# Kernel optimization log

Measured on AMD Instinct MI355X. Metric: run time of the kernel, lower is better.

The kernel has to match this reference:

```python
import jax, jax.numpy as jnp
import numpy as np

EPS_LN = 1e-5

def _layernorm(x, g, b):
    mu = jnp.mean(x, axis=-1, keepdims=True)
    var = jnp.mean((x - mu) ** 2, axis=-1, keepdims=True)
    return (x - mu) * jax.lax.rsqrt(var + EPS_LN) * g + b


def setup_inputs() -> dict:
    B, S, D = 8, 2048, 512
    key = jax.random.key(0)
    ks = jax.random.split(key, 12)
    s = 1.0 / np.sqrt(D)
    inp = {
        "x": jax.random.normal(ks[0], (B, S, D), dtype=jnp.float32),
        "ln1_g": jnp.ones((D,), jnp.float32),
        "ln1_b": jnp.zeros((D,), jnp.float32),
        "ln2_g": jnp.ones((D,), jnp.float32),
        "ln2_b": jnp.zeros((D,), jnp.float32),
        "Wq": jax.random.normal(ks[1], (D, D), jnp.float32) * s,
        "bq": jnp.zeros((D,), jnp.float32),
        "Wk": jax.random.normal(ks[2], (D, D), jnp.float32) * s,
        "bk": jnp.zeros((D,), jnp.float32),
        "Wv": jax.random.normal(ks[3], (D, D), jnp.float32) * s,
        "bv": jnp.zeros((D,), jnp.float32),
        "Wi": jax.random.normal(ks[4], (D, D), jnp.float32) * s,
        "bi": jnp.zeros((D,), jnp.float32),
        "Wf": jax.random.normal(ks[5], (D, D), jnp.float32) * s,
        "bf": jnp.zeros((D,), jnp.float32),
        "Wo": jax.random.normal(ks[6], (D, D), jnp.float32) * s,
        "bo": jnp.zeros((D,), jnp.float32),
        "W1": jax.random.normal(ks[7], (D, 4 * D), jnp.float32) * s,
        "b1": jnp.zeros((4 * D,), jnp.float32),
        "W2": jax.random.normal(ks[8], (4 * D, D), jnp.float32) * (1.0 / np.sqrt(4 * D)),
        "b2": jnp.zeros((D,), jnp.float32),
    }
    return inp


def reference(x, ln1_g, ln1_b, ln2_g, ln2_b, Wq, bq, Wk, bk, Wv, bv,
              Wi, bi, Wf, bf, Wo, bo, W1, b1, W2, b2):
    B, S, D = x.shape
    normed = _layernorm(x, ln1_g, ln1_b)                      # [B,S,D]
    # All projections depend only on x -> batch them over time.
    q = normed @ Wq + bq
    k = (normed @ Wk + bk) / jnp.sqrt(jnp.float32(D))
    v = normed @ Wv + bv
    it = normed @ Wi + bi
    ft = normed @ Wf + bf
    o = jax.nn.sigmoid(normed @ Wo + bo)

    def tm(a):  # time-major [S,B,D]
        return jnp.swapaxes(a, 0, 1)

    def step(carry, xs):
        C, n, m = carry
        q_t, k_t, v_t, it_t, ft_t, o_t = xs
        m_new = jnp.maximum(ft_t + m, it_t)
        i_g = jnp.exp(it_t - m_new)
        f_g = jnp.exp(ft_t + m - m_new)
        # outer(v,k): [B,D,1]*[B,1,D]
        C_new = f_g[..., None] * C + i_g[..., None] * (v_t[:, :, None] * k_t[:, None, :])
        n_new = f_g * n + i_g * k_t
        h = o_t * jnp.einsum('bij,bj->bi', C_new, q_t)
        return (C_new, n_new, m_new), h

    C0 = jnp.zeros((B, D, D), x.dtype)
    n0 = jnp.zeros((B, D), x.dtype)
    m0 = jnp.zeros((B, D), x.dtype)
    (_, _, _), h_seq = jax.lax.scan(step, (C0, n0, m0),
                                    (tm(q), tm(k), tm(v), tm(it), tm(ft), tm(o)))
    h = jnp.swapaxes(h_seq, 0, 1)                             # [B,S,D]

    out = x + h
    ffn_in = _layernorm(out, ln2_g, ln2_b)
    ffn = jax.nn.gelu(ffn_in @ W1 + b1, approximate=False) @ W2 + b2
    return out + ffn
```

## Files before the change

### kernel.cpp

```cpp
#include <hip/hip_runtime.h>
#include <hip/hip_bf16.h>
#include <cstdint>

typedef unsigned short u16;
typedef unsigned int u32;
typedef __attribute__((ext_vector_type(8))) short short8;
typedef __attribute__((ext_vector_type(4))) float f32x4;

#define NB 8
#define NS 2048
#define ND 512
#define NM (NB * NS)
#define CL 64
#define NCH (NS / CL)
static constexpr size_t BSDn = (size_t)NM * ND;
#define KSCALE 0.044194173824159216f

#define OFF_QB ((size_t)0)
#define OFF_KB (BSDn * 2)
#define OFF_KT (BSDn * 4)
#define OFF_VT (BSDn * 6)
#define OFF_OT (BSDn * 8)
#define OFF_IT (BSDn * 10)
#define OFF_FT (BSDn * 14)
#define OFF_G  (BSDn * 18)
#define OFF_AC (BSDn * 18 + ((size_t)2 << 20))
#define OFF_X  (OFF_AC + ((size_t)32 << 20))
#define OFF_UB (OFF_X + ((size_t)16 << 20))
#define OFF_GA (OFF_UB + ((size_t)16 << 20))
#define OFF_END (OFF_GA + ((size_t)1 << 20))

typedef __attribute__((address_space(1))) const u32 gas_u32;
typedef __attribute__((address_space(3))) u32 las_u32;

__device__ __forceinline__ u16 f2bf(float f) {
    u32 i = __builtin_bit_cast(u32, f);
    u32 r = i + 0x7FFFu + ((i >> 16) & 1u);
    return (u16)(r >> 16);
}
__device__ __forceinline__ float bf2f(u16 h) {
    return __builtin_bit_cast(float, (u32)h << 16);
}

__device__ __forceinline__ void lds_barrier() {
    __builtin_amdgcn_sched_barrier(0);
    asm volatile("s_waitcnt lgkmcnt(0)" ::: "memory");
    __builtin_amdgcn_s_barrier();
    __builtin_amdgcn_sched_barrier(0);
}

__global__ __launch_bounds__(256) void wcorr_kernel(
        const float* __restrict__ Wi, const float* __restrict__ Wf,
        u16* __restrict__ WT) {
    int idx = blockIdx.x * 256 + threadIdx.x;
    int n = idx / 1536, k = idx - n * 1536;
    const float* Wp = (n >> 9) ? Wf : Wi;
    int d = n & 511;
    u16 o;
    if (k < 1024) {
        o = f2bf(Wp[(size_t)(k & 511) * 512 + d]);
    } else {
        float w = Wp[(size_t)(k - 1024) * 512 + d];
        o = f2bf(w - bf2f(f2bf(w)));
    }
    WT[idx] = o;
}

__global__ __launch_bounds__(256) void wconv_kernel(const float* __restrict__ W,
        u16* __restrict__ WT, int lk, int N, int total) {
    int idx = blockIdx.x * 256 + threadIdx.x;
    if (idx >= total) return;
    int n = idx >> lk;
    int k = idx & ((1 << lk) - 1);
    WT[idx] = f2bf(W[(size_t)k * N + n]);
}

__global__ __launch_bounds__(256) void bias_concat_kernel(
        const float* b0, const float* b1, const float* b2,
        const float* b3, const float* b4, const float* b5,
        float* __restrict__ ball) {
    int idx = blockIdx.x * 256 + threadIdx.x;
    if (idx >= 3072) return;
    int p = idx >> 9, d = idx & 511;
    float v;
    switch (p) {
        case 0: v = b0[d]; break;
        case 1: v = b1[d]; break;
        case 2: v = b2[d]; break;
        case 3: v = b3[d]; break;
        case 4: v = b4[d]; break;
        default: v = b5[d]; break;
    }
    ball[idx] = v;
}

__global__ __launch_bounds__(256) void ln1_kernel(const float* __restrict__ x,
        const float* __restrict__ g, const float* __restrict__ bb,
        u16* __restrict__ nout) {
    int wave = threadIdx.x >> 6, lane = threadIdx.x & 63;
    size_t row = (size_t)blockIdx.x * 4 + wave;
    const float* xr = x + row * ND + lane * 8;
    float4 a0 = *(const float4*)xr;
    float4 a1 = *(const float4*)(xr + 4);
    float xs[8] = {a0.x, a0.y, a0.z, a0.w, a1.x, a1.y, a1.z, a1.w};
    float s = 0.f;
#pragma unroll
    for (int u = 0; u < 8; ++u) s += xs[u];
#pragma unroll
    for (int off = 32; off; off >>= 1) s += __shfl_xor(s, off);
    float mu = s * (1.0f / ND);
    float ss = 0.f;
#pragma unroll
    for (int u = 0; u < 8; ++u) { xs[u] -= mu; ss += xs[u] * xs[u]; }
#pragma unroll
    for (int off = 32; off; off >>= 1) ss += __shfl_xor(ss, off);
    float rs = rsqrtf(ss * (1.0f / ND) + 1e-5f);
    const float* gp = g + lane * 8;
    const float* bp = bb + lane * 8;
    float4 g0 = *(const float4*)gp, g1 = *(const float4*)(gp + 4);
    float4 c0 = *(const float4*)bp, c1 = *(const float4*)(bp + 4);
    float gg[8] = {g0.x, g0.y, g0.z, g0.w, g1.x, g1.y, g1.z, g1.w};
    float cc[8] = {c0.x, c0.y, c0.z, c0.w, c1.x, c1.y, c1.z, c1.w};
    u32 owh[4], owl[4];
#pragma unroll
    for (int u = 0; u < 4; ++u) {
        float y0 = xs[2 * u] * rs * gg[2 * u] + cc[2 * u];
        float y1 = xs[2 * u + 1] * rs * gg[2 * u + 1] + cc[2 * u + 1];
        u16 h0 = f2bf(y0), h1 = f2bf(y1);
        u16 l0 = f2bf(y0 - bf2f(h0)), l1 = f2bf(y1 - bf2f(h1));
        owh[u] = (u32)h0 | ((u32)h1 << 16);
        owl[u] = (u32)l0 | ((u32)l1 << 16);
    }
    u16* rb = nout + row * 1024;
    *(uint4*)(rb + lane * 8) = make_uint4(owh[0], owh[1], owh[2], owh[3]);
    *(uint4*)(rb + 512 + lane * 8) = make_uint4(owl[0], owl[1], owl[2], owl[3]);
}

__global__ __launch_bounds__(256) void resid_ln2_kernel(const float* __restrict__ x,
        const float* __restrict__ h, const float* __restrict__ g,
        const float* __restrict__ bb, float* __restrict__ outb,
        u16* __restrict__ fin) {
    int wave = threadIdx.x >> 6, lane = threadIdx.x & 63;
    size_t row = (size_t)blockIdx.x * 4 + wave;
    const float* xr = x + row * ND + lane * 8;
    const float* hr = h + row * ND + lane * 8;
    float4 a0 = *(const float4*)xr;
    float4 a1 = *(const float4*)(xr + 4);
    float4 h0 = *(const float4*)hr;
    float4 h1 = *(const float4*)(hr + 4);
    float xs[8] = {a0.x + h0.x, a0.y + h0.y, a0.z + h0.z, a0.w + h0.w,
                   a1.x + h1.x, a1.y + h1.y, a1.z + h1.z, a1.w + h1.w};
    float* orow = outb + row * ND + lane * 8;
    *(float4*)orow = make_float4(xs[0], xs[1], xs[2], xs[3]);
    *(float4*)(orow + 4) = make_float4(xs[4], xs[5], xs[6], xs[7]);
    float s = 0.f;
#pragma unroll
    for (int u = 0; u < 8; ++u) s += xs[u];
#pragma unroll
    for (int off = 32; off; off >>= 1) s += __shfl_xor(s, off);
    float mu = s * (1.0f / ND);
    float ss = 0.f;
#pragma unroll
    for (int u = 0; u < 8; ++u) { xs[u] -= mu; ss += xs[u] * xs[u]; }
#pragma unroll
    for (int off = 32; off; off >>= 1) ss += __shfl_xor(ss, off);
    float rs = rsqrtf(ss * (1.0f / ND) + 1e-5f);
    const float* gp = g + lane * 8;
    const float* bp = bb + lane * 8;
    float4 g0 = *(const float4*)gp, g1 = *(const float4*)(gp + 4);
    float4 c0 = *(const float4*)bp, c1 = *(const float4*)(bp + 4);
    float gg[8] = {g0.x, g0.y, g0.z, g0.w, g1.x, g1.y, g1.z, g1.w};
    float cc[8] = {c0.x, c0.y, c0.z, c0.w, c1.x, c1.y, c1.z, c1.w};
    u32 ow[4];
#pragma unroll
    for (int u = 0; u < 4; ++u) {
        float y0 = xs[2 * u] * rs * gg[2 * u] + cc[2 * u];
        float y1 = xs[2 * u + 1] * rs * gg[2 * u + 1] + cc[2 * u + 1];
        ow[u] = (u32)f2bf(y0) | ((u32)f2bf(y1) << 16);
    }
    *(uint4*)(fin + row * ND + lane * 8) = make_uint4(ow[0], ow[1], ow[2], ow[3]);
}

__global__ __launch_bounds__(256) void gqk_kernel(
        const u16* __restrict__ Qb, const u16* __restrict__ Kb,
        u16* __restrict__ Gm) {
    __shared__ u16 Qs[64][520];
    __shared__ u16 Ks[64][520];
    int tid = threadIdx.x;
    int w = tid >> 6, lane = tid & 63;
    int b = blockIdx.x >> 5, c = blockIdx.x & 31;
    int t0 = c * CL;
    {
        int row = tid >> 2, cb = (tid & 3) * 128;
        const u16* qsrc = Qb + ((size_t)b * NS + t0 + row) * ND + cb;
        const u16* ksrc = Kb + ((size_t)b * NS + t0 + row) * ND + cb;
#pragma unroll
        for (int u = 0; u < 16; ++u) {
            *(short8*)&Qs[row][cb + u * 8] = *(const short8*)(qsrc + u * 8);
            *(short8*)&Ks[row][cb + u * 8] = *(const short8*)(ksrc + u * 8);
        }
    }
    __syncthreads();
    int qw = lane & 15, kg = lane >> 4;
    f32x4 ga[4];
#pragma unroll
    for (int ns = 0; ns < 4; ++ns) ga[ns] = (f32x4){0.f, 0.f, 0.f, 0.f};
    for (int kb = 0; kb < 16; ++kb) {
        short8 aq = *(const short8*)&Qs[(w << 4) + qw][kb * 32 + (kg << 3)];
#pragma unroll
        for (int ns = 0; ns < 4; ++ns) {
            short8 bk = *(const short8*)&Ks[(ns << 4) + qw][kb * 32 + (kg << 3)];
            ga[ns] = __builtin_amdgcn_mfma_f32_16x16x32_bf16(aq, bk, ga[ns], 0, 0, 0);
        }
    }
    u16* gout = Gm + (size_t)(b * NCH + c) * CL * CL;
#pragma unroll
    for (int ns = 0; ns < 4; ++ns) {
#pragma unroll
        for (int rg = 0; rg < 4; ++rg) {
            int t = (w << 4) + (kg << 2) + rg;
            int s = (ns << 4) + qw;
            gout[t * CL + s] = (s <= t) ? f2bf(ga[ns][rg]) : (u16)0;
        }
    }
}

__global__ __launch_bounds__(128) void gates_kernel(
        const float* __restrict__ IT, const float* __restrict__ FT,
        const u16* __restrict__ VT,
        u16* __restrict__ A1g, u16* __restrict__ A2g,
        u16* __restrict__ Ubg, float* __restrict__ gamg) {
    int w = threadIdx.x >> 6, lane = threadIdx.x & 63;
    int rp = blockIdx.x & 7;
    int bl = blockIdx.x >> 3;
    int b = bl >> 5, isl = bl & 31;
    int il = rp * 2 + w;
    int i = (isl << 4) + il;
    size_t rowb = ((size_t)b * ND + i) * NS;
    size_t tb = (size_t)bl * 32 * 1024 + il * 64;
    float mo = 0.f;
    for (int c = 0; c < NCH; ++c) {
        size_t gofs = rowb + c * CL + lane;
        float ft = FT[gofs];
        float it = IT[gofs];
        float vv = bf2f(VT[gofs]);
        float bs = ft;
#pragma unroll
        for (int o = 1; o < 64; o <<= 1) {
            float nv = __shfl_up(bs, o);
            if (lane >= o) bs += nv;
        }
        float e = it - bs;
        float Mv = e;
#pragma unroll
        for (int o = 1; o < 64; o <<= 1) {
            float nv = __shfl_up(Mv, o);
            if (lane >= o) Mv = fmaxf(Mv, nv);
        }
        Mv = fmaxf(Mv, mo);
        float E = __shfl(Mv, 63);
        size_t oofs = tb + (size_t)c * 1024 + lane;
        Ubg[oofs] = f2bf(__expf(e - E) * vv);
        A1g[oofs] = f2bf(__expf(mo - Mv));
        A2g[oofs] = f2bf(__expf(fminf(E - Mv, 80.f)));
        if (lane == 0) gamg[((size_t)bl * 32 + c) * 16 + il] = __expf(mo - E);
        float bs63 = __shfl(bs, 63);
        mo = bs63 + E;
    }
}

__global__ __launch_bounds__(512) void recur_kernel(
        const u16* __restrict__ Qb, const u16* __restrict__ KT,
        const u16* __restrict__ Gm,
        const u16* __restrict__ A1g, const u16* __restrict__ A2g,
        const u16* __restrict__ Ubg, const float* __restrict__ gamg,
        const u16* __restrict__ OT, float* __restrict__ H) {
    __shared__ u16 Chi[2][16][520];
    __shared__ u16 Ubl[2][16][72];
    __shared__ u16 A1l[2][16][66];
    __shared__ u16 A2l[2][16][66];
    __shared__ float gaml[2][16];
    int tid = threadIdx.x;
    int w = tid >> 6, lane = tid & 63;
    int tt = w & 3, half = w >> 2;
    int b = blockIdx.x & 7;
    int isl = blockIdx.x >> 3;
    int i0 = isl << 4;
    int qw = lane & 15, kg = lane >> 4;
    f32x4 cacc[4];
#pragma unroll
    for (int n = 0; n < 4; ++n) cacc[n] = (f32x4){0.f, 0.f, 0.f, 0.f};

    size_t bT = (size_t)b * NS;
    size_t bD = (size_t)b * ND;
    size_t gtile = (size_t)(b * 32 + isl) * 32 * 1024;
    int srow = tid >> 5, spair = (tid & 31) << 1;

    const u16* qpf = Qb + (bT + (tt << 4) + qw) * ND + (kg << 3);
    const u16* kpf = KT + (bD + (w << 6) + qw) * NS + (kg << 3);
    const u16* gpf = Gm + ((size_t)(b * NCH) * CL + (tt << 4) + qw) * CL + (kg << 3);
    const u16* ubp = Ubg + gtile + srow * 64 + spair;
    const u16* a1p = A1g + gtile + srow * 64 + spair;
    const u16* a2p = A2g + gtile + srow * 64 + spair;
    const float* gamp = gamg + (size_t)(b * 32 + isl) * 512 + tid;
    const u16* otp = OT + (bD + i0 + qw) * NS + (tt << 4) + (kg << 2);

    u32 nub = 0, na1 = 0, na2 = 0;
    float ngam = 0.f;
    uint2 nov = make_uint2(0, 0);
    short8 nq[16], nk[8], ng[2];

    auto issue_gates = [&]() {
        nub = *(const u32*)ubp; ubp += 1024;
        na1 = *(const u32*)a1p; a1p += 1024;
        na2 = *(const u32*)a2p; a2p += 1024;
        if (tid < 16) ngam = *gamp;
        gamp += 16;
    };
    auto issue_big = [&]() {
        if (half == 0) {
#pragma unroll
            for (int kk = 0; kk < 16; ++kk)
                nq[kk] = *(const short8*)(qpf + kk * 32);
            ng[0] = *(const short8*)gpf;
            ng[1] = *(const short8*)(gpf + 32);
            nov = *(const uint2*)otp;
        }
        qpf += CL * ND;
        gpf += CL * CL;
        otp += CL;
#pragma unroll
        for (int kb = 0; kb < 2; ++kb)
#pragma unroll
            for (int n = 0; n < 4; ++n)
                nk[kb * 4 + n] = *(const short8*)(kpf + (size_t)(n << 4) * NS + kb * 32);
        kpf += CL;
    };

    issue_gates();
    issue_big();
    for (int c = 0; c < NCH; ++c) {
        int buf = c & 1;
        int t0 = c * CL;
        u32 cub = nub, ca1 = na1, ca2 = na2;
        float cgam = ngam;
        uint2 cov = nov;
        if (c + 1 < NCH) issue_gates();

        *(u32*)&Ubl[buf][srow][spair] = cub;
        *(u32*)&A1l[buf][srow][spair] = ca1;
        *(u32*)&A2l[buf][srow][spair] = ca2;
        if (tid < 16) gaml[buf][tid] = cgam;
#pragma unroll
        for (int n = 0; n < 4; ++n) {
            int j = (w << 6) + (n << 4) + qw;
#pragma unroll
            for (int rg = 0; rg < 4; ++rg)
                Chi[buf][(kg << 2) + rg][j] = f2bf(cacc[n][rg]);
        }
        lds_barrier();

        f32x4 qc0 = (f32x4){0.f, 0.f, 0.f, 0.f};
        f32x4 qc1 = (f32x4){0.f, 0.f, 0.f, 0.f};
        f32x4 pin = (f32x4){0.f, 0.f, 0.f, 0.f};
        if (half == 0) {
#pragma unroll
            for (int kk = 0; kk < 8; ++kk) {
                short8 b0 = *(const short8*)&Chi[buf][qw][(2 * kk) * 32 + (kg << 3)];
                short8 b1 = *(const short8*)&Chi[buf][qw][(2 * kk + 1) * 32 + (kg << 3)];
                qc0 = __builtin_amdgcn_mfma_f32_16x16x32_bf16(nq[2 * kk], b0, qc0, 0, 0, 0);
                qc1 = __builtin_amdgcn_mfma_f32_16x16x32_bf16(nq[2 * kk + 1], b1, qc1, 0, 0, 0);
            }
#pragma unroll
            for (int kb = 0; kb < 2; ++kb) {
                short8 bu = *(const short8*)&Ubl[buf][qw][kb * 32 + (kg << 3)];
                pin = __builtin_amdgcn_mfma_f32_16x16x32_bf16(ng[kb], bu, pin, 0, 0, 0);
            }
        }
        {
            float g[4];
#pragma unroll
            for (int rg = 0; rg < 4; ++rg) g[rg] = gaml[buf][(kg << 2) + rg];
#pragma unroll
            for (int n = 0; n < 4; ++n) {
#pragma unroll
                for (int rg = 0; rg < 4; ++rg) cacc[n][rg] *= g[rg];
            }
#pragma unroll
            for (int kb = 0; kb < 2; ++kb) {
                short8 au = *(const short8*)&Ubl[buf][qw][kb * 32 + (kg << 3)];
#pragma unroll
                for (int n = 0; n < 4; ++n)
                    cacc[n] = __builtin_amdgcn_mfma_f32_16x16x32_bf16(
                            au, nk[kb * 4 + n], cacc[n], 0, 0, 0);
            }
        }
        float a1v[4], a2v[4];
        if (half == 0) {
#pragma unroll
            for (int rg = 0; rg < 4; ++rg) {
                int tl = (tt << 4) + (kg << 2) + rg;
                a1v[rg] = bf2f(A1l[buf][qw][tl]);
                a2v[rg] = bf2f(A2l[buf][qw][tl]);
            }
        }
        if (c + 1 < NCH) issue_big();
        if (half == 0) {
            float ov[4];
            ov[0] = bf2f((u16)(cov.x & 0xffff));
            ov[1] = bf2f((u16)(cov.x >> 16));
            ov[2] = bf2f((u16)(cov.y & 0xffff));
            ov[3] = bf2f((u16)(cov.y >> 16));
#pragma unroll
            for (int rg = 0; rg < 4; ++rg) {
                int tl = (tt << 4) + (kg << 2) + rg;
                float qc = qc0[rg] + qc1[rg];
                H[(bT + t0 + tl) * ND + i0 + qw] = ov[rg] * (a1v[rg] * qc + a2v[rg] * pin[rg]);
            }
        }
    }
}

template <int MODE>
__global__ __launch_bounds__(256) void gemm_kernel(
        const u16* __restrict__ A, const u16* __restrict__ BT,
        int M, int N, int K, int lda, int ldb, int kwrap,
        const float* __restrict__ bias,
        char* __restrict__ pb,
        float* __restrict__ outf, u16* __restrict__ outh,
        const float* __restrict__ resid) {
    __shared__ u16 As[2][128 * 32];
    __shared__ u16 Bs[2][128 * 32];
    int tid = threadIdx.x;
    int wave = tid >> 6, lane = tid & 63;
    int wm = wave >> 1, wn = wave & 1;
    int m0 = blockIdx.y * 128;
    int n0 = blockIdx.x * 128;

    f32x4 acc[4][4];
#pragma unroll
    for (int fi = 0; fi < 4; ++fi)
#pragma unroll
        for (int fj = 0; fj < 4; ++fj)
            acc[fi][fj] = (f32x4){0.f, 0.f, 0.f, 0.f};

    int srow = lane >> 2;
    int slot = lane & 3;
    int r0s = wave * 32 + srow;
    int gs0 = (slot ^ ((r0s >> 1) & 3)) << 3;
    int gs1 = (slot ^ (((r0s + 16) >> 1) & 3)) << 3;
    const u16* Ag0 = A + (size_t)(m0 + r0s) * lda + gs0;
    const u16* Ag1 = A + (size_t)(m0 + r0s + 16) * lda + gs1;
    const u16* Bg0 = BT + (size_t)(n0 + r0s) * ldb + gs0;
    const u16* Bg1 = BT + (size_t)(n0 + r0s + 16) * ldb + gs1;
    int wl0 = wave * 32 * 32;
    int wl1 = wl0 + 16 * 32;

    int fr = lane & 15, kb = lane >> 4;
    int ra[4], rb4[4], sa[4], sb[4];
#pragma unroll
    for (int f = 0; f < 4; ++f) {
        ra[f] = wm * 64 + f * 16 + fr;
        rb4[f] = wn * 64 + f * 16 + fr;
        sa[f] = ra[f] * 32 + ((kb ^ ((ra[f] >> 1) & 3)) << 3);
        sb[f] = rb4[f] * 32 + ((kb ^ ((rb4[f] >> 1) & 3)) << 3);
    }

    int nk = K >> 5;
    __builtin_amdgcn_global_load_lds((gas_u32*)Ag0, (las_u32*)(&As[0][wl0]), 16, 0, 0);
    __builtin_amdgcn_global_load_lds((gas_u32*)Ag1, (las_u32*)(&As[0][wl1]), 16, 0, 0);
    __builtin_amdgcn_global_load_lds((gas_u32*)Bg0, (las_u32*)(&Bs[0][wl0]), 16, 0, 0);
    __builtin_amdgcn_global_load_lds((gas_u32*)Bg1, (las_u32*)(&Bs[0][wl1]), 16, 0, 0);
    __syncthreads();
#pragma unroll 2
    for (int t = 0; t < nk; ++t) {
        int cur = t & 1;
        if (t + 1 < nk) {
            int k0 = (t + 1) << 5;
            int ak0 = k0 - (k0 >= kwrap ? kwrap : 0);
            __builtin_amdgcn_global_load_lds((gas_u32*)(Ag0 + ak0), (las_u32*)(&As[cur ^ 1][wl0]), 16, 0, 0);
            __builtin_amdgcn_global_load_lds((gas_u32*)(Ag1 + ak0), (las_u32*)(&As[cur ^ 1][wl1]), 16, 0, 0);
            __builtin_amdgcn_global_load_lds((gas_u32*)(Bg0 + k0), (las_u32*)(&Bs[cur ^ 1][wl0]), 16, 0, 0);
            __builtin_amdgcn_global_load_lds((gas_u32*)(Bg1 + k0), (las_u32*)(&Bs[cur ^ 1][wl1]), 16, 0, 0);
        }
        short8 fa[4], fb[4];
#pragma unroll
        for (int f = 0; f < 4; ++f) {
            fa[f] = *(const short8*)(&As[cur][sa[f]]);
            fb[f] = *(const short8*)(&Bs[cur][sb[f]]);
        }
#pragma unroll
        for (int fi = 0; fi < 4; ++fi)
#pragma unroll
            for (int fj = 0; fj < 4; ++fj)
                acc[fi][fj] = __builtin_amdgcn_mfma_f32_16x16x32_bf16(
                        fa[fi], fb[fj], acc[fi][fj], 0, 0, 0);
        __syncthreads();
    }

    int rbase = (lane >> 4) * 4;
    int cbase = n0 + wn * 64 + (lane & 15);
#pragma unroll
    for (int fi = 0; fi < 4; ++fi) {
        int r0 = m0 + wm * 64 + fi * 16 + rbase;
#pragma unroll
        for (int fj = 0; fj < 4; ++fj) {
            int col = cbase + fj * 16;
            if (MODE == 0) {
                int p = col >> 9, d = col & 511;
                float bv_ = bias[col];
                float w0 = acc[fi][fj][0] + bv_;
                float w1 = acc[fi][fj][1] + bv_;
                float w2 = acc[fi][fj][2] + bv_;
                float w3 = acc[fi][fj][3] + bv_;
                size_t tb = ((size_t)(r0 >> 11) * ND + d) * NS + (r0 & 2047);
                if (p == 0) {
                    u16* q = (u16*)(pb + OFF_QB);
                    q[(size_t)(r0 + 0) * ND + d] = f2bf(w0);
                    q[(size_t)(r0 + 1) * ND + d] = f2bf(w1);
                    q[(size_t)(r0 + 2) * ND + d] = f2bf(w2);
                    q[(size_t)(r0 + 3) * ND + d] = f2bf(w3);
                } else if (p == 1) {
                    float s0 = w0 * KSCALE, s1 = w1 * KSCALE;
                    float s2 = w2 * KSCALE, s3 = w3 * KSCALE;
                    u16* kbuf = (u16*)(pb + OFF_KB);
                    kbuf[(size_t)(r0 + 0) * ND + d] = f2bf(s0);
                    kbuf[(size_t)(r0 + 1) * ND + d] = f2bf(s1);
                    kbuf[(size_t)(r0 + 2) * ND + d] = f2bf(s2);
                    kbuf[(size_t)(r0 + 3) * ND + d] = f2bf(s3);
                    uint2 wv = make_uint2((u32)f2bf(s0) | ((u32)f2bf(s1) << 16),
                                          (u32)f2bf(s2) | ((u32)f2bf(s3) << 16));
                    *(uint2*)((u16*)(pb + OFF_KT) + tb) = wv;
                } else if (p == 2) {
                    uint2 wv = make_uint2((u32)f2bf(w0) | ((u32)f2bf(w1) << 16),
                                          (u32)f2bf(w2) | ((u32)f2bf(w3) << 16));
                    *(uint2*)((u16*)(pb + OFF_VT) + tb) = wv;
                } else {
                    float s0 = 1.0f / (1.0f + __expf(-w0));
                    float s1 = 1.0f / (1.0f + __expf(-w1));
                    float s2 = 1.0f / (1.0f + __expf(-w2));
                    float s3 = 1.0f / (1.0f + __expf(-w3));
                    uint2 wv = make_uint2((u32)f2bf(s0) | ((u32)f2bf(s1) << 16),
                                          (u32)f2bf(s2) | ((u32)f2bf(s3) << 16));
                    *(uint2*)((u16*)(pb + OFF_OT) + tb) = wv;
                }
            } else if (MODE == 3) {
                int p = col >> 9, d = col & 511;
                float bv_ = bias[col];
                float w0 = acc[fi][fj][0] + bv_;
                float w1 = acc[fi][fj][1] + bv_;
                float w2 = acc[fi][fj][2] + bv_;
                float w3 = acc[fi][fj][3] + bv_;
                size_t tb = ((size_t)(r0 >> 11) * ND + d) * NS + (r0 & 2047);
                float* dst = (float*)(pb + (p == 0 ? OFF_IT : OFF_FT));
                *(float4*)(dst + tb) = make_float4(w0, w1, w2, w3);
            } else {
#pragma unroll
                for (int r = 0; r < 4; ++r) {
                    int row = r0 + r;
                    float v = acc[fi][fj][r];
                    if (MODE == 1) {
                        float val = v + bias[col];
                        val = 0.5f * val * (1.0f + erff(val * 0.70710678118654752f));
                        outh[(size_t)row * N + col] = f2bf(val);
                    } else {
                        float val = v + bias[col] + resid[(size_t)row * ND + col];
                        outf[(size_t)row * ND + col] = val;
                    }
                }
            }
        }
    }
}

extern "C" void kernel_launch(void* const* d_in, const int* in_sizes, int n_in,
                              void* d_out, int out_size, void* d_ws, size_t ws_size,
                              hipStream_t stream) {
    const float* x    = (const float*)d_in[0];
    const float* ln1g = (const float*)d_in[1];
    const float* ln1b = (const float*)d_in[2];
    const float* ln2g = (const float*)d_in[3];
    const float* ln2b = (const float*)d_in[4];
    const float* Wq = (const float*)d_in[5];
    const float* bq = (const float*)d_in[6];
    const float* Wk = (const float*)d_in[7];
    const float* bk = (const float*)d_in[8];
    const float* Wv = (const float*)d_in[9];
    const float* bv = (const float*)d_in[10];
    const float* Wi = (const float*)d_in[11];
    const float* bi = (const float*)d_in[12];
    const float* Wf = (const float*)d_in[13];
    const float* bfp = (const float*)d_in[14];
    const float* Wo = (const float*)d_in[15];
    const float* bo = (const float*)d_in[16];
    const float* W1 = (const float*)d_in[17];
    const float* b1 = (const float*)d_in[18];
    const float* W2 = (const float*)d_in[19];
    const float* b2 = (const float*)d_in[20];
    float* out = (float*)d_out;

    char* ws = (char*)d_ws;
    size_t off = 0;
    u16* W4T    = (u16*)(ws + off); off += (size_t)2048 * 512 * 2;
    u16* WcT    = (u16*)(ws + off); off += (size_t)1024 * 1536 * 2;
    u16* W1T    = (u16*)(ws + off); off += (size_t)2048 * 512 * 2;
    u16* W2T    = (u16*)(ws + off); off += (size_t)512 * 2048 * 2;
    float* ball = (float*)(ws + off); off += 3072 * 4;
    off = (off + 255) & ~(size_t)255;
    char* U = ws + off;
    u16*   Acorr = (u16*)(U + OFF_AC);
    float* Hbuf  = (float*)(U + OFF_AC);
    u16* ffnin = (u16*)U;
    u16* Gbuf  = (u16*)(U + OFF_KB);
    u16* A1g   = (u16*)(U + OFF_KB);
    u16* A2g   = (u16*)(U + OFF_X);
    u16* Ubg   = (u16*)(U + OFF_UB);
    float* gamg = (float*)(U + OFF_GA);
    size_t needed = (size_t)(U - ws) + OFF_END;
    if (ws_size < needed) return;

    wconv_kernel<<<1024, 256, 0, stream>>>(Wq, W4T, 9, 512, 512 * 512);
    wconv_kernel<<<1024, 256, 0, stream>>>(Wk, W4T + (size_t)512 * 512, 9, 512, 512 * 512);
    wconv_kernel<<<1024, 256, 0, stream>>>(Wv, W4T + (size_t)2 * 512 * 512, 9, 512, 512 * 512);
    wconv_kernel<<<1024, 256, 0, stream>>>(Wo, W4T + (size_t)3 * 512 * 512, 9, 512, 512 * 512);
    wcorr_kernel<<<(1024 * 1536) / 256, 256, 0, stream>>>(Wi, Wf, WcT);
    wconv_kernel<<<4096, 256, 0, stream>>>(W1, W1T, 9, 2048, 2048 * 512);
    wconv_kernel<<<4096, 256, 0, stream>>>(W2, W2T, 11, 512, 512 * 2048);
    bias_concat_kernel<<<12, 256, 0, stream>>>(bq, bk, bv, bo, bi, bfp, ball);

    ln1_kernel<<<NM / 4, 256, 0, stream>>>(x, ln1g, ln1b, Acorr);

    gemm_kernel<0><<<dim3(2048 / 128, NM / 128), 256, 0, stream>>>(
            Acorr, W4T, NM, 2048, 512, 1024, 512, 1 << 30, ball,
            U, nullptr, nullptr, nullptr);
    gemm_kernel<3><<<dim3(1024 / 128, NM / 128), 256, 0, stream>>>(
            Acorr, WcT, NM, 1024, 1536, 1024, 1536, 1024, ball + 2048,
            U, nullptr, nullptr, nullptr);

    gqk_kernel<<<NB * NCH, 256, 0, stream>>>(
            (const u16*)(U + OFF_QB), (const u16*)(U + OFF_KB), (u16*)(U + OFF_G));

    gates_kernel<<<NB * 32 * 8, 128, 0, stream>>>(
            (const float*)(U + OFF_IT), (const float*)(U + OFF_FT),
            (const u16*)(U + OFF_VT), A1g, A2g, Ubg, gamg);

    recur_kernel<<<NB * 32, 512, 0, stream>>>(
            (const u16*)(U + OFF_QB), (const u16*)(U + OFF_KT), (const u16*)(U + OFF_G),
            A1g, A2g, Ubg, gamg, (const u16*)(U + OFF_OT), Hbuf);

    resid_ln2_kernel<<<NM / 4, 256, 0, stream>>>(x, Hbuf, ln2g, ln2b, out, ffnin);

    gemm_kernel<1><<<dim3(2048 / 128, NM / 128), 256, 0, stream>>>(
            ffnin, W1T, NM, 2048, 512, 512, 512, 1 << 30, b1,
            nullptr, nullptr, Gbuf, nullptr);

    gemm_kernel<2><<<dim3(512 / 128, NM / 128), 256, 0, stream>>>(
            Gbuf, W2T, NM, 512, 2048, 2048, 2048, 1 << 30, b2,
            nullptr, out, nullptr, out);

    (void)in_sizes; (void)n_in; (void)out_size; (void)ws_size;
}
```

Measured before the change: 569.6 us.

## Double the recurrence chunk length to 128 and add an off-diagonal QK block kernel

Each recurrence step now covers 128 timesteps instead of 64, halving the number of sequential chunk steps and barriers in recur_kernel. All 8 waves now compute query outputs, where before only half of them did. A new gqkoff_kernel precomputes the off-diagonal 64x64 Q·K block between the two halves of each 128-chunk, and the gates kernel runs two 64-lane scans per chunk. In exchange it adds a kernel launch and extra workspace, and drops the previous software prefetch of the next chunk's Q, K and G data, so those loads are no longer overlapped with compute.

```diff
diff --git a/kernel.cpp b/kernel.cpp
--- a/kernel.cpp
+++ b/kernel.cpp
@@ -13,6 +13,8 @@
 #define NM (NB * NS)
 #define CL 64
 #define NCH (NS / CL)
+#define CL2 128
+#define NCH2 (NS / CL2)
 static constexpr size_t BSDn = (size_t)NM * ND;
 #define KSCALE 0.044194173824159216f
 
@@ -24,7 +26,8 @@
 #define OFF_IT (BSDn * 10)
 #define OFF_FT (BSDn * 14)
 #define OFF_G  (BSDn * 18)
-#define OFF_AC (BSDn * 18 + ((size_t)2 << 20))
+#define OFF_GO (BSDn * 18 + ((size_t)2 << 20))
+#define OFF_AC (BSDn * 18 + ((size_t)3 << 20))
 #define OFF_X  (OFF_AC + ((size_t)32 << 20))
 #define OFF_UB (OFF_X + ((size_t)16 << 20))
 #define OFF_GA (OFF_UB + ((size_t)16 << 20))
@@ -225,6 +228,50 @@
     }
 }
 
+__global__ __launch_bounds__(256) void gqkoff_kernel(
+        const u16* __restrict__ Qb, const u16* __restrict__ Kb,
+        u16* __restrict__ Go) {
+    __shared__ u16 Qs[64][520];
+    __shared__ u16 Ks[64][520];
+    int tid = threadIdx.x;
+    int w = tid >> 6, lane = tid & 63;
+    int b = blockIdx.x >> 4, c = blockIdx.x & 15;
+    int t0q = c * CL2 + 64, t0k = c * CL2;
+    {
+        int row = tid >> 2, cb = (tid & 3) * 128;
+        const u16* qsrc = Qb + ((size_t)b * NS + t0q + row) * ND + cb;
+        const u16* ksrc = Kb + ((size_t)b * NS + t0k + row) * ND + cb;
+#pragma unroll
+        for (int u = 0; u < 16; ++u) {
+            *(short8*)&Qs[row][cb + u * 8] = *(const short8*)(qsrc + u * 8);
+            *(short8*)&Ks[row][cb + u * 8] = *(const short8*)(ksrc + u * 8);
+        }
+    }
+    __syncthreads();
+    int qw = lane & 15, kg = lane >> 4;
+    f32x4 ga[4];
+#pragma unroll
+    for (int ns = 0; ns < 4; ++ns) ga[ns] = (f32x4){0.f, 0.f, 0.f, 0.f};
+    for (int kb = 0; kb < 16; ++kb) {
+        short8 aq = *(const short8*)&Qs[(w << 4) + qw][kb * 32 + (kg << 3)];
+#pragma unroll
+        for (int ns = 0; ns < 4; ++ns) {
+            short8 bk = *(const short8*)&Ks[(ns << 4) + qw][kb * 32 + (kg << 3)];
+            ga[ns] = __builtin_amdgcn_mfma_f32_16x16x32_bf16(aq, bk, ga[ns], 0, 0, 0);
+        }
+    }
+    u16* gout = Go + (size_t)(b * NCH2 + c) * CL * CL;
+#pragma unroll
+    for (int ns = 0; ns < 4; ++ns) {
+#pragma unroll
+        for (int rg = 0; rg < 4; ++rg) {
+            int t = (w << 4) + (kg << 2) + rg;
+            int s = (ns << 4) + qw;
+            gout[t * CL + s] = f2bf(ga[ns][rg]);
+        }
+    }
+}
+
 __global__ __launch_bounds__(128) void gates_kernel(
         const float* __restrict__ IT, const float* __restrict__ FT,
         const u16* __restrict__ VT,
@@ -237,52 +284,71 @@
     int il = rp * 2 + w;
     int i = (isl << 4) + il;
     size_t rowb = ((size_t)b * ND + i) * NS;
-    size_t tb = (size_t)bl * 32 * 1024 + il * 64;
+    size_t tb = (size_t)bl * 32768 + il * 128;
     float mo = 0.f;
-    for (int c = 0; c < NCH; ++c) {
-        size_t gofs = rowb + c * CL + lane;
-        float ft = FT[gofs];
-        float it = IT[gofs];
-        float vv = bf2f(VT[gofs]);
-        float bs = ft;
+    for (int c = 0; c < NCH2; ++c) {
+        size_t g0 = rowb + c * CL2 + lane;
+        float ft0 = FT[g0], it0 = IT[g0], v0 = bf2f(VT[g0]);
+        float ft1 = FT[g0 + 64], it1 = IT[g0 + 64], v1 = bf2f(VT[g0 + 64]);
+        float bs0 = ft0;
 #pragma unroll
         for (int o = 1; o < 64; o <<= 1) {
-            float nv = __shfl_up(bs, o);
-            if (lane >= o) bs += nv;
-        }
-        float e = it - bs;
-        float Mv = e;
+            float nv = __shfl_up(bs0, o);
+            if (lane >= o) bs0 += nv;
+        }
+        float e0 = it0 - bs0;
+        float M0 = e0;
 #pragma unroll
         for (int o = 1; o < 64; o <<= 1) {
-            float nv = __shfl_up(Mv, o);
-            if (lane >= o) Mv = fmaxf(Mv, nv);
-        }
-        Mv = fmaxf(Mv, mo);
-        float E = __shfl(Mv, 63);
-        size_t oofs = tb + (size_t)c * 1024 + lane;
-        Ubg[oofs] = f2bf(__expf(e - E) * vv);
-        A1g[oofs] = f2bf(__expf(mo - Mv));
-        A2g[oofs] = f2bf(__expf(fminf(E - Mv, 80.f)));
-        if (lane == 0) gamg[((size_t)bl * 32 + c) * 16 + il] = __expf(mo - E);
-        float bs63 = __shfl(bs, 63);
-        mo = bs63 + E;
+            float nv = __shfl_up(M0, o);
+            if (lane >= o) M0 = fmaxf(M0, nv);
+        }
+        M0 = fmaxf(M0, mo);
+        float M0t = __shfl(M0, 63);
+        float bs0t = __shfl(bs0, 63);
+        float bs1 = ft1;
+#pragma unroll
+        for (int o = 1; o < 64; o <<= 1) {
+            float nv = __shfl_up(bs1, o);
+            if (lane >= o) bs1 += nv;
+        }
+        bs1 += bs0t;
+        float e1 = it1 - bs1;
+        float M1 = e1;
+#pragma unroll
+        for (int o = 1; o < 64; o <<= 1) {
+            float nv = __shfl_up(M1, o);
+            if (lane >= o) M1 = fmaxf(M1, nv);
+        }
+        M1 = fmaxf(M1, M0t);
+        float E = __shfl(M1, 63);
+        float bst = __shfl(bs1, 63);
+        size_t oofs = tb + (size_t)c * 2048 + lane;
+        Ubg[oofs] = f2bf(__expf(e0 - E) * v0);
+        A1g[oofs] = f2bf(__expf(mo - M0));
+        A2g[oofs] = f2bf(__expf(fminf(E - M0, 80.f)));
+        Ubg[oofs + 64] = f2bf(__expf(e1 - E) * v1);
+        A1g[oofs + 64] = f2bf(__expf(mo - M1));
+        A2g[oofs + 64] = f2bf(__expf(fminf(E - M1, 80.f)));
+        if (lane == 0) gamg[((size_t)bl * NCH2 + c) * 16 + il] = __expf(mo - E);
+        mo = bst + E;
     }
 }
 
 __global__ __launch_bounds__(512) void recur_kernel(
         const u16* __restrict__ Qb, const u16* __restrict__ KT,
-        const u16* __restrict__ Gm,
+        const u16* __restrict__ Gd, const u16* __restrict__ Go,
         const u16* __restrict__ A1g, const u16* __restrict__ A2g,
         const u16* __restrict__ Ubg, const float* __restrict__ gamg,
         const u16* __restrict__ OT, float* __restrict__ H) {
     __shared__ u16 Chi[2][16][520];
-    __shared__ u16 Ubl[2][16][72];
-    __shared__ u16 A1l[2][16][66];
-    __shared__ u16 A2l[2][16][66];
+    __shared__ u16 Ubl[2][16][136];
+    __shared__ u16 A1l[2][16][136];
+    __shared__ u16 A2l[2][16][136];
     __shared__ float gaml[2][16];
     int tid = threadIdx.x;
     int w = tid >> 6, lane = tid & 63;
-    int tt = w & 3, half = w >> 2;
+    int hb = w >> 2, tl16 = w & 3;
     int b = blockIdx.x & 7;
     int isl = blockIdx.x >> 3;
     int i0 = isl << 4;
@@ -293,63 +359,63 @@
 
     size_t bT = (size_t)b * NS;
     size_t bD = (size_t)b * ND;
-    size_t gtile = (size_t)(b * 32 + isl) * 32 * 1024;
-    int srow = tid >> 5, spair = (tid & 31) << 1;
-
-    const u16* qpf = Qb + (bT + (tt << 4) + qw) * ND + (kg << 3);
-    const u16* kpf = KT + (bD + (w << 6) + qw) * NS + (kg << 3);
-    const u16* gpf = Gm + ((size_t)(b * NCH) * CL + (tt << 4) + qw) * CL + (kg << 3);
-    const u16* ubp = Ubg + gtile + srow * 64 + spair;
-    const u16* a1p = A1g + gtile + srow * 64 + spair;
-    const u16* a2p = A2g + gtile + srow * 64 + spair;
-    const float* gamp = gamg + (size_t)(b * 32 + isl) * 512 + tid;
-    const u16* otp = OT + (bD + i0 + qw) * NS + (tt << 4) + (kg << 2);
-
-    u32 nub = 0, na1 = 0, na2 = 0;
+    size_t gt2 = (size_t)(b * 32 + isl) * 32768;
+    int grow = tid >> 5;
+    int gquad = (tid & 31) << 2;
+
+    const u16* qpf = Qb + (bT + w * 16 + qw) * ND + (kg << 3);
+    const u16* kpf = KT + (bD + w * 64 + qw) * NS + (kg << 3);
+    const u16* gdp = Gd + ((size_t)(b * 32 + hb) * 4096)
+                     + (size_t)(tl16 * 16 + qw) * 64 + (kg << 3);
+    const u16* gop = Go + ((size_t)(b * 16) * 4096)
+                     + (size_t)(tl16 * 16 + qw) * 64 + (kg << 3);
+    const u16* ubp = Ubg + gt2 + grow * 128 + gquad;
+    const u16* a1p = A1g + gt2 + grow * 128 + gquad;
+    const u16* a2p = A2g + gt2 + grow * 128 + gquad;
+    const float* gamp = gamg + (size_t)(b * 32 + isl) * (NCH2 * 16) + tid;
+    const u16* otp = OT + (bD + i0 + qw) * NS + w * 16 + (kg << 2);
+
+    uint2 nub = make_uint2(0, 0), na1 = make_uint2(0, 0), na2 = make_uint2(0, 0);
     float ngam = 0.f;
-    uint2 nov = make_uint2(0, 0);
-    short8 nq[16], nk[8], ng[2];
-
     auto issue_gates = [&]() {
-        nub = *(const u32*)ubp; ubp += 1024;
-        na1 = *(const u32*)a1p; a1p += 1024;
-        na2 = *(const u32*)a2p; a2p += 1024;
+        nub = *(const uint2*)ubp; ubp += 2048;
+        na1 = *(const uint2*)a1p; a1p += 2048;
+        na2 = *(const uint2*)a2p; a2p += 2048;
         if (tid < 16) ngam = *gamp;
         gamp += 16;
     };
-    auto issue_big = [&]() {
-        if (half == 0) {
-#pragma unroll
-            for (int kk = 0; kk < 16; ++kk)
-                nq[kk] = *(const short8*)(qpf + kk * 32);
-            ng[0] = *(const short8*)gpf;
-            ng[1] = *(const short8*)(gpf + 32);
-            nov = *(const uint2*)otp;
-        }
-        qpf += CL * ND;
-        gpf += CL * CL;
-        otp += CL;
-#pragma unroll
-        for (int kb = 0; kb < 2; ++kb)
+    issue_gates();
+
+    for (int c = 0; c < NCH2; ++c) {
+        int buf = c & 1;
+        int t0 = c * CL2;
+        short8 nq[16], nk[16], ngd[2], ngo[2];
+#pragma unroll
+        for (int kk = 0; kk < 16; ++kk) nq[kk] = *(const short8*)(qpf + kk * 32);
+        qpf += CL2 * ND;
+#pragma unroll
+        for (int kb = 0; kb < 4; ++kb)
 #pragma unroll
             for (int n = 0; n < 4; ++n)
                 nk[kb * 4 + n] = *(const short8*)(kpf + (size_t)(n << 4) * NS + kb * 32);
-        kpf += CL;
-    };
-
-    issue_gates();
-    issue_big();
-    for (int c = 0; c < NCH; ++c) {
-        int buf = c & 1;
-        int t0 = c * CL;
-        u32 cub = nub, ca1 = na1, ca2 = na2;
+        kpf += CL2;
+        ngd[0] = *(const short8*)gdp;
+        ngd[1] = *(const short8*)(gdp + 32);
+        gdp += 2 * 4096;
+        if (hb == 1) {
+            ngo[0] = *(const short8*)gop;
+            ngo[1] = *(const short8*)(gop + 32);
+        }
+        gop += 4096;
+        uint2 cov = *(const uint2*)otp;
+        otp += CL2;
+        uint2 cub = nub, ca1 = na1, ca2 = na2;
         float cgam = ngam;
-        uint2 cov = nov;
-        if (c + 1 < NCH) issue_gates();
-
-        *(u32*)&Ubl[buf][srow][spair] = cub;
-        *(u32*)&A1l[buf][srow][spair] = ca1;
-        *(u32*)&A2l[buf][srow][spair] = ca2;
+        if (c + 1 < NCH2) issue_gates();
+
+        *(uint2*)&Ubl[buf][grow][gquad] = cub;
+        *(uint2*)&A1l[buf][grow][gquad] = ca1;
+        *(uint2*)&A2l[buf][grow][gquad] = ca2;
         if (tid < 16) gaml[buf][tid] = cgam;
 #pragma unroll
         for (int n = 0; n < 4; ++n) {
@@ -362,19 +428,30 @@
 
         f32x4 qc0 = (f32x4){0.f, 0.f, 0.f, 0.f};
         f32x4 qc1 = (f32x4){0.f, 0.f, 0.f, 0.f};
+#pragma unroll
+        for (int kk = 0; kk < 8; ++kk) {
+            short8 b0 = *(const short8*)&Chi[buf][qw][(2 * kk) * 32 + (kg << 3)];
+            short8 b1_ = *(const short8*)&Chi[buf][qw][(2 * kk + 1) * 32 + (kg << 3)];
+            qc0 = __builtin_amdgcn_mfma_f32_16x16x32_bf16(nq[2 * kk], b0, qc0, 0, 0, 0);
+            qc1 = __builtin_amdgcn_mfma_f32_16x16x32_bf16(nq[2 * kk + 1], b1_, qc1, 0, 0, 0);
+        }
         f32x4 pin = (f32x4){0.f, 0.f, 0.f, 0.f};
-        if (half == 0) {
-#pragma unroll
-            for (int kk = 0; kk < 8; ++kk) {
-                short8 b0 = *(const short8*)&Chi[buf][qw][(2 * kk) * 32 + (kg << 3)];
-                short8 b1 = *(const short8*)&Chi[buf][qw][(2 * kk + 1) * 32 + (kg << 3)];
-                qc0 = __builtin_amdgcn_mfma_f32_16x16x32_bf16(nq[2 * kk], b0, qc0, 0, 0, 0);
-                qc1 = __builtin_amdgcn_mfma_f32_16x16x32_bf16(nq[2 * kk + 1], b1, qc1, 0, 0, 0);
-            }
+        if (hb == 0) {
 #pragma unroll
             for (int kb = 0; kb < 2; ++kb) {
                 short8 bu = *(const short8*)&Ubl[buf][qw][kb * 32 + (kg << 3)];
-                pin = __builtin_amdgcn_mfma_f32_16x16x32_bf16(ng[kb], bu, pin, 0, 0, 0);
+                pin = __builtin_amdgcn_mfma_f32_16x16x32_bf16(ngd[kb], bu, pin, 0, 0, 0);
+            }
+        } else {
+#pragma unroll
+            for (int kb = 0; kb < 2; ++kb) {
+                short8 bu = *(const short8*)&Ubl[buf][qw][kb * 32 + (kg << 3)];
+                pin = __builtin_amdgcn_mfma_f32_16x16x32_bf16(ngo[kb], bu, pin, 0, 0, 0);
+            }
+#pragma unroll
+            for (int kb = 0; kb < 2; ++kb) {
+                short8 bu = *(const short8*)&Ubl[buf][qw][64 + kb * 32 + (kg << 3)];
+                pin = __builtin_amdgcn_mfma_f32_16x16x32_bf16(ngd[kb], bu, pin, 0, 0, 0);
             }
         }
         {
@@ -387,7 +464,7 @@
                 for (int rg = 0; rg < 4; ++rg) cacc[n][rg] *= g[rg];
             }
 #pragma unroll
-            for (int kb = 0; kb < 2; ++kb) {
+            for (int kb = 0; kb < 4; ++kb) {
                 short8 au = *(const short8*)&Ubl[buf][qw][kb * 32 + (kg << 3)];
 #pragma unroll
                 for (int n = 0; n < 4; ++n)
@@ -395,17 +472,7 @@
                             au, nk[kb * 4 + n], cacc[n], 0, 0, 0);
             }
         }
-        float a1v[4], a2v[4];
-        if (half == 0) {
-#pragma unroll
-            for (int rg = 0; rg < 4; ++rg) {
-                int tl = (tt << 4) + (kg << 2) + rg;
-                a1v[rg] = bf2f(A1l[buf][qw][tl]);
-                a2v[rg] = bf2f(A2l[buf][qw][tl]);
-            }
-        }
-        if (c + 1 < NCH) issue_big();
-        if (half == 0) {
+        {
             float ov[4];
             ov[0] = bf2f((u16)(cov.x & 0xffff));
             ov[1] = bf2f((u16)(cov.x >> 16));
@@ -413,9 +480,11 @@
             ov[3] = bf2f((u16)(cov.y >> 16));
 #pragma unroll
             for (int rg = 0; rg < 4; ++rg) {
-                int tl = (tt << 4) + (kg << 2) + rg;
+                int tl = w * 16 + (kg << 2) + rg;
+                float a1v = bf2f(A1l[buf][qw][tl]);
+                float a2v = bf2f(A2l[buf][qw][tl]);
                 float qc = qc0[rg] + qc1[rg];
-                H[(bT + t0 + tl) * ND + i0 + qw] = ov[rg] * (a1v[rg] * qc + a2v[rg] * pin[rg]);
+                H[(bT + t0 + tl) * ND + i0 + qw] = ov[rg] * (a1v * qc + a2v * pin[rg]);
             }
         }
     }
@@ -639,13 +708,16 @@
 
     gqk_kernel<<<NB * NCH, 256, 0, stream>>>(
             (const u16*)(U + OFF_QB), (const u16*)(U + OFF_KB), (u16*)(U + OFF_G));
+    gqkoff_kernel<<<NB * NCH2, 256, 0, stream>>>(
+            (const u16*)(U + OFF_QB), (const u16*)(U + OFF_KB), (u16*)(U + OFF_GO));
 
     gates_kernel<<<NB * 32 * 8, 128, 0, stream>>>(
             (const float*)(U + OFF_IT), (const float*)(U + OFF_FT),
             (const u16*)(U + OFF_VT), A1g, A2g, Ubg, gamg);
 
     recur_kernel<<<NB * 32, 512, 0, stream>>>(
-            (const u16*)(U + OFF_QB), (const u16*)(U + OFF_KT), (const u16*)(U + OFF_G),
+            (const u16*)(U + OFF_QB), (const u16*)(U + OFF_KT),
+            (const u16*)(U + OFF_G), (const u16*)(U + OFF_GO),
             A1g, A2g, Ubg, gamg, (const u16*)(U + OFF_OT), Hbuf);
 
     resid_ln2_kernel<<<NM / 4, 256, 0, stream>>>(x, Hbuf, ln2g, ln2b, out, ffnin);
```

Result: no change. 569.3 us (-0.0%).
